# Kernel tuning notes

Measured on AMD Instinct MI355X. Metric: run time of the kernel, lower is better.

## Reference

```python
import jax, jax.numpy as jnp
import numpy as np

B = 8192      # batch size (first half RGB samples, second half IR samples)
C = 2048      # feature dim, hard-coded by nn.Linear(2048, 1)
N_RGB = 4     # rgb cams: ids 0..3
L = 6         # total camera nodes (4 rgb + 2 ir)


def setup_inputs() -> dict:
    key = jax.random.key(0)
    k1, k2, k3, k4, k5, k6 = jax.random.split(key, 6)
    x = jax.random.normal(k1, (B, C), dtype=jnp.float32)
    # first half of batch comes from RGB cams, second half from IR cams (modal == 0 layout)
    cams_rgb = jax.random.randint(k2, (B // 2,), 0, N_RGB)
    cams_ir = jax.random.randint(k3, (B // 2,), N_RGB, L)
    cams = jnp.concatenate([cams_rgb, cams_ir]).astype(jnp.int32)
    att_w = jax.random.normal(k4, (L, C), dtype=jnp.float32) * 0.02  # nn.Linear(2048,1) weights per cam
    att_b = jax.random.normal(k5, (L,), dtype=jnp.float32) * 0.02
    running_mean = jax.random.normal(k6, (L, C), dtype=jnp.float32) * 0.1
    return {"x": x, "cams": cams, "step": 0, "modal": 0,
            "att_w": att_w, "att_b": att_b, "running_mean": running_mean}


def _gen_adj(graph):
    # D = diag(rowsum^-0.5); adj = (graph @ D).T @ D  ==  D[:,None] * graph.T * D[None,:]
    D = jnp.power(graph.sum(axis=1), -0.5)
    return D[:, None] * graph.T * D[None, :]


def reference(x, cams, step, modal, att_w, att_b, running_mean):
    Bv, Cv = x.shape
    Lv = running_mean.shape[0]
    half = Bv // 2
    dt = x.dtype

    # ---- adjacency construction (modal == 0 branch) ----
    is_rgb_cam = jnp.arange(Lv) < N_RGB                        # [L] camera modality
    samp_first_half = jnp.arange(Bv) < half                    # [B]
    # adj[:B//2,:B//2]=1 and adj[B//2:,B//2:]=1 (identity diag already covered)
    bb = (samp_first_half[:, None] == samp_first_half[None, :]).astype(dt)   # [B,B]
    # sample from cam c connects to every cam node of the OTHER modality
    cross = (is_rgb_cam[:, None] != is_rgb_cam[None, :]).astype(dt)          # [L,L]
    bc = cross[cams]                                                          # [B,L]
    cc = jnp.eye(Lv, dtype=dt)                                                # cam-node diag from eye(B+L)
    graph = jnp.concatenate([
        jnp.concatenate([bb, bc], axis=1),
        jnp.concatenate([bc.T, cc], axis=1),
    ], axis=0)                                                                # [B+L, B+L]
    adj = _gen_adj(graph)

    # ---- per-camera attention-weighted pooling (training branch) ----
    # score_n = x_n @ w_{cam_n} + b_{cam_n}
    scores = jnp.einsum('bc,bc->b', x, att_w[cams]) + att_b[cams]             # [B]
    denom = jax.ops.segment_sum(scores, cams, num_segments=Lv)                # per-cam sum
    w = scores / denom[cams]                                                  # weight / weight.sum()
    cam_center = jax.ops.segment_sum(x * w[:, None], cams, num_segments=Lv)   # [L,C]
    # only cams present in the batch get overwritten; absent cams keep running mean
    counts = jax.ops.segment_sum(jnp.ones((Bv,), dtype=dt), cams, num_segments=Lv)
    tail = jnp.where((counts > 0)[:, None], cam_center, running_mean)         # [L,C]

    x_out = jnp.concatenate([x, tail], axis=0)                                # [B+L, C]
    return x_out, adj
```

## Files before the change

kernel.cpp:

```cpp
#include <hip/hip_runtime.h>

#define B      8192
#define C      2048
#define C4     (C / 4)
#define HALF   4096
#define L      6
#define NRGB   4
#define BT     (B + L)
#define XOUT_ELEMS ((size_t)BT * C)

#define NBLK   256
#define RPB    32

#define ROWF2  4099
#define SPANF2 2048

typedef float v2f __attribute__((ext_vector_type(2)));

__device__ __forceinline__ void fill_row_main(const int i, const int tid,
                                              v2f* __restrict__ a2full) {
  const float ds_rgb = rsqrtf(4098.f);
  const float ds_ir  = rsqrtf(4100.f);
  const float dc     = rsqrtf(4097.f);
  float v0, v1;
  if (i < HALF)          { v0 = ds_rgb * ds_rgb; v1 = 0.f; }
  else if (i < B)        { v0 = 0.f;             v1 = ds_ir * ds_ir; }
  else if (i - B < NRGB) { v0 = 0.f;             v1 = dc * ds_ir; }
  else                   { v0 = dc * ds_rgb;     v1 = 0.f; }
  v2f* __restrict__ a2 = a2full + (size_t)i * ROWF2;
  const v2f w0 = {v0, v0};
  const v2f w1 = {v1, v1};
  #pragma unroll
  for (int k = 0; k < 8; ++k)
    __builtin_nontemporal_store(w0, &a2[k * 256 + tid]);
  #pragma unroll
  for (int k = 0; k < 8; ++k)
    __builtin_nontemporal_store(w1, &a2[SPANF2 + k * 256 + tid]);
}

__device__ __forceinline__ void fill_row_tail6(const int r, v2f* __restrict__ a2full) {
  const float ds_rgb = rsqrtf(4098.f);
  const float ds_ir  = rsqrtf(4100.f);
  const float dc     = rsqrtf(4097.f);
  v2f t0, t1, t2;
  if (r < HALF) {
    const float a = ds_rgb * dc;
    t0 = (v2f){0.f, 0.f}; t1 = (v2f){0.f, 0.f}; t2 = (v2f){a, a};
  } else if (r < B) {
    const float a = ds_ir * dc;
    t0 = (v2f){a, a}; t1 = (v2f){a, a}; t2 = (v2f){0.f, 0.f};
  } else {
    const int l = r - B;
    const float d2 = dc * dc;
    t0 = (v2f){l == 0 ? d2 : 0.f, l == 1 ? d2 : 0.f};
    t1 = (v2f){l == 2 ? d2 : 0.f, l == 3 ? d2 : 0.f};
    t2 = (v2f){l == 4 ? d2 : 0.f, l == 5 ? d2 : 0.f};
  }
  v2f* __restrict__ a2 = a2full + (size_t)r * ROWF2 + 2 * SPANF2;
  __builtin_nontemporal_store(t0, &a2[0]);
  __builtin_nontemporal_store(t1, &a2[1]);
  __builtin_nontemporal_store(t2, &a2[2]);
}

__global__ __launch_bounds__(256) void k_main(
    const float* __restrict__ x, const int* __restrict__ cams,
    const float* __restrict__ att_w, const float* __restrict__ att_b,
    float* __restrict__ xout, float* __restrict__ partials,
    float* __restrict__ statpart, float* __restrict__ adj, const int i0) {
  const int bx  = blockIdx.x;
  const int tid = threadIdx.x;

  if (bx >= NBLK) {
    v2f* a2full = (v2f*)adj;
    const int nrows = BT - i0;
    const int fb = bx - NBLK;
    if (fb < nrows) {
      fill_row_main(i0 + fb, tid, a2full);
    } else {
      const int r = i0 + (fb - nrows) * 256 + tid;
      if (r < BT) fill_row_tail6(r, a2full);
    }
    return;
  }

  __shared__ float ls[RPB];
  __shared__ int   lcam[RPB];
  __shared__ float sden[L];
  __shared__ int   scnt[L];
  const int wv = tid >> 6;
  const int ln = tid & 63;
  const int r0 = bx * RPB;

  if (tid < L)   { sden[tid] = 0.f; scnt[tid] = 0; }
  if (tid < RPB) lcam[tid] = cams[r0 + tid];
  __syncthreads();

  const float4* __restrict__ x4 = (const float4*)x;
  const float4* __restrict__ w4 = (const float4*)att_w;
  float4* __restrict__ o4       = (float4*)xout;

  for (int j = 0; j < 8; ++j) {
    const int rl  = wv * 8 + j;
    const int cam = lcam[rl];
    const size_t xb = (size_t)(r0 + rl) * C4;
    const size_t wb = (size_t)cam * C4;
    float acc = 0.f;
    #pragma unroll
    for (int k = 0; k < 8; ++k) {
      const float4 xx = x4[xb + k * 64 + ln];
      const float4 ww = w4[wb + k * 64 + ln];
      acc += xx.x * ww.x + xx.y * ww.y + xx.z * ww.z + xx.w * ww.w;
    }
    #pragma unroll
    for (int off = 32; off > 0; off >>= 1) acc += __shfl_xor(acc, off, 64);
    if (ln == 0) {
      const float s = acc + att_b[cam];
      ls[rl] = s;
      atomicAdd(&sden[cam], s);
      atomicAdd(&scnt[cam], 1);
    }
  }
  __syncthreads();

  float4 a[L][2];
  #pragma unroll
  for (int l = 0; l < L; ++l) {
    a[l][0] = make_float4(0.f, 0.f, 0.f, 0.f);
    a[l][1] = make_float4(0.f, 0.f, 0.f, 0.f);
  }
  for (int rl = 0; rl < RPB; ++rl) {
    const int   cam = __builtin_amdgcn_readfirstlane(lcam[rl]);
    const float s   = ls[rl];
    const size_t xb = (size_t)(r0 + rl) * C4;
    const float4 xa = x4[xb + tid];
    const float4 xc = x4[xb + 256 + tid];
    o4[xb + tid]       = xa;
    o4[xb + 256 + tid] = xc;
    float4 va, vc;
    va.x = xa.x * s; va.y = xa.y * s; va.z = xa.z * s; va.w = xa.w * s;
    vc.x = xc.x * s; vc.y = xc.y * s; vc.z = xc.z * s; vc.w = xc.w * s;
    #define ACC(l) { a[l][0].x+=va.x; a[l][0].y+=va.y; a[l][0].z+=va.z; a[l][0].w+=va.w; \
                     a[l][1].x+=vc.x; a[l][1].y+=vc.y; a[l][1].z+=vc.z; a[l][1].w+=vc.w; }
    if      (cam == 0) ACC(0)
    else if (cam == 1) ACC(1)
    else if (cam == 2) ACC(2)
    else if (cam == 3) ACC(3)
    else if (cam == 4) ACC(4)
    else               ACC(5)
    #undef ACC
  }
  float4* __restrict__ p4 = (float4*)partials + (size_t)bx * (L * C4);
  #pragma unroll
  for (int l = 0; l < L; ++l) {
    p4[l * C4 + tid]       = a[l][0];
    p4[l * C4 + 256 + tid] = a[l][1];
  }
  if (tid < L)           statpart[bx * 12 + tid] = sden[tid];
  else if (tid < 2 * L)  statpart[bx * 12 + tid] = (float)scnt[tid - L];
}

__global__ __launch_bounds__(256) void k_tail(
    const float* __restrict__ partials, const float* __restrict__ statpart,
    const float* __restrict__ running_mean, float* __restrict__ xout) {
  const int l    = blockIdx.x / 32;
  const int cg   = blockIdx.x % 32;
  const int tid  = threadIdx.x;
  const int wv   = tid >> 6;
  const int ln   = tid & 63;

  float d = statpart[tid * 12 + l];
  float n = statpart[tid * 12 + 6 + l];
  #pragma unroll
  for (int off = 32; off > 0; off >>= 1) {
    d += __shfl_xor(d, off, 64);
    n += __shfl_xor(n, off, 64);
  }
  __shared__ float sdn[8];
  if (ln == 0) { sdn[wv] = d; sdn[4 + wv] = n; }

  const int c4i  = tid & 15;
  const int gs   = tid >> 4;
  const int col4 = cg * 16 + c4i;
  const float4* __restrict__ p4 = (const float4*)partials;
  float4 acc = make_float4(0.f, 0.f, 0.f, 0.f);
  for (int t = 0; t < NBLK / 16; ++t) {
    const int g = gs + t * 16;
    const float4 v = p4[((size_t)g * L + l) * C4 + col4];
    acc.x += v.x; acc.y += v.y; acc.z += v.z; acc.w += v.w;
  }
  __shared__ float4 red[16][16];
  red[gs][c4i] = acc;
  __syncthreads();
  if (tid < 16) {
    const float denom = sdn[0] + sdn[1] + sdn[2] + sdn[3];
    const float count = sdn[4] + sdn[5] + sdn[6] + sdn[7];
    const int myc4 = cg * 16 + tid;
    float4 t = make_float4(0.f, 0.f, 0.f, 0.f);
    #pragma unroll
    for (int g = 0; g < 16; ++g) {
      const float4 v = red[g][tid];
      t.x += v.x; t.y += v.y; t.z += v.z; t.w += v.w;
    }
    float4 o;
    if (count > 0.f) {
      const float inv = 1.0f / denom;
      o.x = t.x * inv; o.y = t.y * inv; o.z = t.z * inv; o.w = t.w * inv;
    } else {
      o = ((const float4*)running_mean)[(size_t)l * C4 + myc4];
    }
    ((float4*)xout)[((size_t)B + l) * C4 + myc4] = o;
  }
}

__global__ __launch_bounds__(256) void k_fill_head(float* __restrict__ adj, const int i0) {
  const int bx  = blockIdx.x;
  const int tid = threadIdx.x;
  v2f* a2full = (v2f*)adj;
  if (bx < i0) {
    fill_row_main(bx, tid, a2full);
  } else {
    const int r = (bx - i0) * 256 + tid;
    if (r < i0) fill_row_tail6(r, a2full);
  }
}

extern "C" void kernel_launch(void* const* d_in, const int* in_sizes, int n_in,
                              void* d_out, int out_size, void* d_ws, size_t ws_size,
                              hipStream_t stream) {
  const float* x            = (const float*)d_in[0];
  const int*   cams         = (const int*)d_in[1];
  const float* att_w        = (const float*)d_in[4];
  const float* att_b        = (const float*)d_in[5];
  const float* running_mean = (const float*)d_in[6];

  float* xout = (float*)d_out;
  float* adj  = xout + XOUT_ELEMS;

  const size_t PART_FLOATS = (size_t)NBLK * L * C;
  const size_t NEED_BYTES  = (PART_FLOATS + NBLK * 12) * sizeof(float);

  if (ws_size >= NEED_BYTES) {
    float* partials = (float*)d_ws;
    float* statpart = partials + PART_FLOATS;
    const int grid = NBLK + BT + (BT + 255) / 256;
    k_main<<<grid, 256, 0, stream>>>(x, cams, att_w, att_b, xout,
                                     partials, statpart, adj, 0);
    k_tail<<<32 * L, 256, 0, stream>>>(partials, statpart, running_mean, xout);
  } else {
    const int i0 = 400;
    float* partials = adj;
    float* statpart = adj + PART_FLOATS;
    const int nrows = BT - i0;
    const int grid  = NBLK + nrows + (nrows + 255) / 256;
    k_main<<<grid, 256, 0, stream>>>(x, cams, att_w, att_b, xout,
                                     partials, statpart, adj, i0);
    k_tail     <<<32 * L, 256, 0, stream>>>(partials, statpart, running_mean, xout);
    k_fill_head<<<i0 + (i0 + 255) / 256, 256, 0, stream>>>(adj, i0);
  }
}
```

Measured before the change: 78.38 us.

## Fuse score dot-product into single pass over x with register-resident weights

The score computation and the weighted accumulation previously made two separate passes over each block's 32 rows of x. They now run as one pass that handles four rows at a time. All six per-camera weight vectors are held in registers, and the row dot products are reduced across the four waves through double-buffered shared memory. This reads x once instead of twice, at the cost of a __syncthreads per group of four rows and extra register pressure from the 12 float4 weight values.

```diff
diff --git a/kernel.cpp b/kernel.cpp
--- a/kernel.cpp
+++ b/kernel.cpp
@@ -83,44 +83,33 @@
     return;
   }
 
-  __shared__ float ls[RPB];
   __shared__ int   lcam[RPB];
+  __shared__ float lbias[RPB];
+  __shared__ float pl[2][4][4];
   __shared__ float sden[L];
   __shared__ int   scnt[L];
   const int wv = tid >> 6;
   const int ln = tid & 63;
   const int r0 = bx * RPB;
 
-  if (tid < L)   { sden[tid] = 0.f; scnt[tid] = 0; }
-  if (tid < RPB) lcam[tid] = cams[r0 + tid];
+  if (tid < L) { sden[tid] = 0.f; scnt[tid] = 0; }
+  if (tid < RPB) {
+    const int c = cams[r0 + tid];
+    lcam[tid]  = c;
+    lbias[tid] = att_b[c];
+  }
   __syncthreads();
 
   const float4* __restrict__ x4 = (const float4*)x;
   const float4* __restrict__ w4 = (const float4*)att_w;
   float4* __restrict__ o4       = (float4*)xout;
 
-  for (int j = 0; j < 8; ++j) {
-    const int rl  = wv * 8 + j;
-    const int cam = lcam[rl];
-    const size_t xb = (size_t)(r0 + rl) * C4;
-    const size_t wb = (size_t)cam * C4;
-    float acc = 0.f;
-    #pragma unroll
-    for (int k = 0; k < 8; ++k) {
-      const float4 xx = x4[xb + k * 64 + ln];
-      const float4 ww = w4[wb + k * 64 + ln];
-      acc += xx.x * ww.x + xx.y * ww.y + xx.z * ww.z + xx.w * ww.w;
-    }
-    #pragma unroll
-    for (int off = 32; off > 0; off >>= 1) acc += __shfl_xor(acc, off, 64);
-    if (ln == 0) {
-      const float s = acc + att_b[cam];
-      ls[rl] = s;
-      atomicAdd(&sden[cam], s);
-      atomicAdd(&scnt[cam], 1);
-    }
-  }
-  __syncthreads();
+  const float4 wA0 = w4[0 * C4 + tid], wC0 = w4[0 * C4 + 256 + tid];
+  const float4 wA1 = w4[1 * C4 + tid], wC1 = w4[1 * C4 + 256 + tid];
+  const float4 wA2 = w4[2 * C4 + tid], wC2 = w4[2 * C4 + 256 + tid];
+  const float4 wA3 = w4[3 * C4 + tid], wC3 = w4[3 * C4 + 256 + tid];
+  const float4 wA4 = w4[4 * C4 + tid], wC4 = w4[4 * C4 + 256 + tid];
+  const float4 wA5 = w4[5 * C4 + tid], wC5 = w4[5 * C4 + 256 + tid];
 
   float4 a[L][2];
   #pragma unroll
@@ -128,33 +117,77 @@
     a[l][0] = make_float4(0.f, 0.f, 0.f, 0.f);
     a[l][1] = make_float4(0.f, 0.f, 0.f, 0.f);
   }
-  for (int rl = 0; rl < RPB; ++rl) {
-    const int   cam = __builtin_amdgcn_readfirstlane(lcam[rl]);
-    const float s   = ls[rl];
-    const size_t xb = (size_t)(r0 + rl) * C4;
-    const float4 xa = x4[xb + tid];
-    const float4 xc = x4[xb + 256 + tid];
-    o4[xb + tid]       = xa;
-    o4[xb + 256 + tid] = xc;
-    float4 va, vc;
-    va.x = xa.x * s; va.y = xa.y * s; va.z = xa.z * s; va.w = xa.w * s;
-    vc.x = xc.x * s; vc.y = xc.y * s; vc.z = xc.z * s; vc.w = xc.w * s;
-    #define ACC(l) { a[l][0].x+=va.x; a[l][0].y+=va.y; a[l][0].z+=va.z; a[l][0].w+=va.w; \
-                     a[l][1].x+=vc.x; a[l][1].y+=vc.y; a[l][1].z+=vc.z; a[l][1].w+=vc.w; }
-    if      (cam == 0) ACC(0)
-    else if (cam == 1) ACC(1)
-    else if (cam == 2) ACC(2)
-    else if (cam == 3) ACC(3)
-    else if (cam == 4) ACC(4)
-    else               ACC(5)
-    #undef ACC
-  }
+
+  for (int cc = 0; cc < RPB / 4; ++cc) {
+    float4 xa[4], xc[4];
+    float  p[4];
+    int    cm[4];
+    #pragma unroll
+    for (int q = 0; q < 4; ++q) {
+      const int rl = cc * 4 + q;
+      cm[q] = lcam[rl];
+      const size_t xb = (size_t)(r0 + rl) * C4;
+      xa[q] = x4[xb + tid];
+      xc[q] = x4[xb + 256 + tid];
+      o4[xb + tid]       = xa[q];
+      o4[xb + 256 + tid] = xc[q];
+      float4 wa, wc;
+      const int c = cm[q];
+      if      (c == 0) { wa = wA0; wc = wC0; }
+      else if (c == 1) { wa = wA1; wc = wC1; }
+      else if (c == 2) { wa = wA2; wc = wC2; }
+      else if (c == 3) { wa = wA3; wc = wC3; }
+      else if (c == 4) { wa = wA4; wc = wC4; }
+      else             { wa = wA5; wc = wC5; }
+      p[q] = xa[q].x * wa.x + xa[q].y * wa.y + xa[q].z * wa.z + xa[q].w * wa.w
+           + xc[q].x * wc.x + xc[q].y * wc.y + xc[q].z * wc.z + xc[q].w * wc.w;
+    }
+    #pragma unroll
+    for (int q = 0; q < 4; ++q) {
+      float v = p[q];
+      #pragma unroll
+      for (int off = 32; off > 0; off >>= 1) v += __shfl_xor(v, off, 64);
+      if (ln == 0) pl[cc & 1][q][wv] = v;
+    }
+    __syncthreads();
+    float s[4];
+    #pragma unroll
+    for (int q = 0; q < 4; ++q)
+      s[q] = pl[cc & 1][q][0] + pl[cc & 1][q][1] + pl[cc & 1][q][2] + pl[cc & 1][q][3]
+           + lbias[cc * 4 + q];
+    if (tid == 0) {
+      #pragma unroll
+      for (int q = 0; q < 4; ++q) {
+        atomicAdd(&sden[cm[q]], s[q]);
+        atomicAdd(&scnt[cm[q]], 1);
+      }
+    }
+    #pragma unroll
+    for (int q = 0; q < 4; ++q) {
+      const float sq = s[q];
+      float4 va, vc;
+      va.x = xa[q].x * sq; va.y = xa[q].y * sq; va.z = xa[q].z * sq; va.w = xa[q].w * sq;
+      vc.x = xc[q].x * sq; vc.y = xc[q].y * sq; vc.z = xc[q].z * sq; vc.w = xc[q].w * sq;
+      #define ACC(l) { a[l][0].x+=va.x; a[l][0].y+=va.y; a[l][0].z+=va.z; a[l][0].w+=va.w; \
+                       a[l][1].x+=vc.x; a[l][1].y+=vc.y; a[l][1].z+=vc.z; a[l][1].w+=vc.w; }
+      const int c = cm[q];
+      if      (c == 0) ACC(0)
+      else if (c == 1) ACC(1)
+      else if (c == 2) ACC(2)
+      else if (c == 3) ACC(3)
+      else if (c == 4) ACC(4)
+      else             ACC(5)
+      #undef ACC
+    }
+  }
+
   float4* __restrict__ p4 = (float4*)partials + (size_t)bx * (L * C4);
   #pragma unroll
   for (int l = 0; l < L; ++l) {
     p4[l * C4 + tid]       = a[l][0];
     p4[l * C4 + 256 + tid] = a[l][1];
   }
+  __syncthreads();
   if (tid < L)           statpart[bx * 12 + tid] = sden[tid];
   else if (tid < 2 * L)  statpart[bx * 12 + tid] = (float)scnt[tid - L];
 }
```

Result: faster. 71.84 us (-8.3%).
